# Optimization experiments

Hardware: AMD Instinct MI355X
Metric: run time of the kernel (lower is better)

Reference implementation:

```python
import jax, jax.numpy as jnp
import numpy as np

N_NODES = 50000  # 4 node types x 12500
N_PER = 12500
E = 600000
H = 128
IN_DIMS = [128, 128, 64, 64]


def setup_inputs() -> dict:
    key = jax.random.key(0)
    ks = jax.random.split(key, 16)
    inp = {}
    for i, d in enumerate(IN_DIMS):
        inp[f"feat{i}"] = jax.random.normal(ks[i], (N_PER, d), dtype=jnp.float32)
        # xavier_normal-ish init, gain 1.414
        std = 1.414 * np.sqrt(2.0 / (d + H))
        inp[f"W_fc{i}"] = jax.random.normal(ks[4 + i], (d, H), dtype=jnp.float32) * std
        inp[f"b_fc{i}"] = jnp.zeros((H,), dtype=jnp.float32)
    inp["src"] = jax.random.randint(ks[8], (E,), 0, N_NODES, dtype=jnp.int32)
    inp["dst"] = jax.random.randint(ks[9], (E,), 0, N_NODES, dtype=jnp.int32)
    inp["e_feat"] = jax.random.randint(ks[10], (E,), 0, 36, dtype=jnp.int32)
    inp["b_g0"] = jnp.zeros((H,), dtype=jnp.float32)  # GraphConv layer0 (weight=False, bias)
    inp["W_g1"] = jax.random.normal(ks[11], (H, H), dtype=jnp.float32) * np.sqrt(1.0 / H)
    inp["b_g1"] = jnp.zeros((H,), dtype=jnp.float32)
    return inp


def _degree_norms(src, dst):
    ones = jnp.ones((src.shape[0],), dtype=jnp.float32)
    deg_out = jax.ops.segment_sum(ones, src, num_segments=N_NODES)
    deg_in = jax.ops.segment_sum(ones, dst, num_segments=N_NODES)
    # DGL norm='both': D_out^{-1/2} on src side, D_in^{-1/2} on dst side (clamp 0-degree)
    out_norm = jax.lax.rsqrt(jnp.maximum(deg_out, 1.0))
    in_norm = jax.lax.rsqrt(jnp.maximum(deg_in, 1.0))
    return out_norm, in_norm


def _gcn_aggregate(h, src, dst, out_norm, in_norm):
    m = (h * out_norm[:, None])[src]                      # [E, H] gather
    agg = jax.ops.segment_sum(m, dst, num_segments=N_NODES)
    return agg * in_norm[:, None]


def reference(feat0, feat1, feat2, feat3,
              W_fc0, b_fc0, W_fc1, b_fc1, W_fc2, b_fc2, W_fc3, b_fc3,
              src, dst, e_feat, b_g0, W_g1, b_g1):
    # per-node-type linear projections, then concat along node dim
    h = jnp.concatenate([
        feat0 @ W_fc0 + b_fc0,
        feat1 @ W_fc1 + b_fc1,
        feat2 @ W_fc2 + b_fc2,
        feat3 @ W_fc3 + b_fc3,
    ], axis=0)  # [N_NODES, H]

    out_norm, in_norm = _degree_norms(src, dst)
    # GraphConv layer 0: weight=False, bias, activation (dropout p=0 -> identity)
    h = jax.nn.relu(_gcn_aggregate(h, src, dst, out_norm, in_norm) + b_g0)
    # GraphConv layer 1: aggregate, then linear weight + bias, activation
    h = jax.nn.relu(_gcn_aggregate(h, src, dst, out_norm, in_norm) @ W_g1 + b_g1)

    e = e_feat.astype(jnp.float32)  # e_feat.reshape(-1,1).float() in original
    # forward graph: msg = ft + sum_{r in 0..4} where(e==r, ft, 0) = ft * (1 + 1{e in 0..4})
    w_fwd = 1.0 + sum((e == float(r)).astype(jnp.float32) for r in (0, 1, 2, 3, 4))
    agg_a = jax.ops.segment_sum(h[src] * w_fwd[:, None], dst, num_segments=N_NODES)
    # transpose graph (reversed edges, same e): msg = sum_{r in {6,14,30}} where(e==r, ft, 0)
    w_bwd = sum((e == float(r)).astype(jnp.float32) for r in (6, 14, 30))
    agg_b = jax.ops.segment_sum(h[dst] * w_bwd[:, None], src, num_segments=N_NODES)
    return agg_a + agg_b
```

## Files before the change

kernel.cpp:

```cpp
#include <hip/hip_runtime.h>
#include <hip/hip_bf16.h>

#define N_NODES 50000
#define N_PER   12500
#define E_EDGES 600000
#define HDIM    128

#define NBLK_FC    ((N_PER + 63) / 64)
#define NBLK_NODE  ((N_NODES + 255) / 256)
#define MASK31  0x7fffffff

#define HQD 64
#define HSL_D (E_EDGES / HQD)
#define NBLK_DB (HQD * 4)

typedef __attribute__((ext_vector_type(8))) short bfrag;
typedef __attribute__((ext_vector_type(4))) float ffrag;

__device__ __forceinline__ unsigned short f2bf(float f) {
    union { float f; unsigned u; } x; x.f = f;
    unsigned r = x.u + 0x7fffu + ((x.u >> 16) & 1u);
    return (unsigned short)(r >> 16);
}
__device__ __forceinline__ float lo_bf(unsigned v) { return __uint_as_float(v << 16); }
__device__ __forceinline__ float hi_bf(unsigned v) { return __uint_as_float(v & 0xffff0000u); }
__device__ __forceinline__ unsigned pack2(float a, float b) {
    return (unsigned)f2bf(a) | ((unsigned)f2bf(b) << 16);
}
__device__ __forceinline__ float onrm_of(int deg) {
    return rsqrtf(fmaxf((float)deg, 1.0f));
}

__device__ __forceinline__ void acc8_add(float* acc, uint4 v) {
    acc[0] += lo_bf(v.x); acc[1] += hi_bf(v.x);
    acc[2] += lo_bf(v.y); acc[3] += hi_bf(v.y);
    acc[4] += lo_bf(v.z); acc[5] += hi_bf(v.z);
    acc[6] += lo_bf(v.w); acc[7] += hi_bf(v.w);
}
__device__ __forceinline__ void acc8_addw(float* acc, uint4 v, float w) {
    acc[0] += lo_bf(v.x) * w; acc[1] += hi_bf(v.x) * w;
    acc[2] += lo_bf(v.y) * w; acc[3] += hi_bf(v.y) * w;
    acc[4] += lo_bf(v.z) * w; acc[5] += hi_bf(v.z) * w;
    acc[6] += lo_bf(v.w) * w; acc[7] += hi_bf(v.w) * w;
}

__global__ __launch_bounds__(1024) void prep_kernel(
    const float* __restrict__ W0, const float* __restrict__ W1,
    const float* __restrict__ W2, const float* __restrict__ W3,
    const float* __restrict__ Wg,
    const int* __restrict__ src, const int* __restrict__ dst,
    const int* __restrict__ ef,
    unsigned short* __restrict__ Wp,
    unsigned short* __restrict__ partialS,
    unsigned short* __restrict__ partialD,
    unsigned char*  __restrict__ partialB) {
    __shared__ unsigned hist[N_PER];
    int b = blockIdx.x;
    if (b < NBLK_DB) {
        const int q = b >> 2;
        const int p = b & 3;
        const int g0 = p * N_PER;
        for (int j = threadIdx.x; j < N_PER; j += 1024) hist[j] = 0;
        __syncthreads();
        const int e0 = q * HSL_D;
        for (int i = e0 + threadIdx.x; i < e0 + HSL_D; i += 1024) {
            int d = dst[i], t = ef[i], s = src[i];
            unsigned rd = (unsigned)(d - g0);
            if (rd < (unsigned)N_PER) atomicAdd(&hist[rd], 1u);
            unsigned rs = (unsigned)(s - g0);
            if (rs < (unsigned)N_PER) {
                unsigned inc = 0x10000u
                             + ((t == 6 || t == 14 || t == 30) ? 0x400u : 0u);
                atomicAdd(&hist[rs], inc);
            }
        }
        __syncthreads();
        for (int j = threadIdx.x; j < N_PER; j += 1024) {
            unsigned h = hist[j];
            partialD[(size_t)q * N_NODES + g0 + j] = (unsigned short)(h & 0x3FFu);
            partialB[(size_t)q * N_NODES + g0 + j] = (unsigned char)((h >> 10) & 0x3Fu);
            partialS[(size_t)q * N_NODES + g0 + j] = (unsigned short)(h >> 16);
        }
    } else {
        int tid = (b - NBLK_DB) * 1024 + threadIdx.x;
        const float* W; int D, base, off;
        if      (tid < 2048) { W = W0; D = 128; base = 0;    off = 0;     }
        else if (tid < 4096) { W = W1; D = 128; base = 2048; off = 16384; }
        else if (tid < 5120) { W = W2; D = 64;  base = 4096; off = 32768; }
        else if (tid < 6144) { W = W3; D = 64;  base = 5120; off = 40960; }
        else                 { W = Wg; D = 128; base = 6144; off = 49152; }
        int t2 = tid - base;
        int KT = D / 32;
        int l = t2 & 63;
        int tt = t2 >> 6;
        int kt = tt % KT, n0 = tt / KT;
        int n = n0 * 16 + (l & 15);
        int kb = kt * 32 + (l >> 4) * 8;
#pragma unroll
        for (int j = 0; j < 8; ++j)
            Wp[(size_t)off + (size_t)t2 * 8 + j] = f2bf(W[(size_t)(kb + j) * 128 + n]);
    }
}

__global__ __launch_bounds__(256) void plane_prefix_kernel(
    unsigned short* __restrict__ partialD, unsigned char* __restrict__ partialB,
    const unsigned short* __restrict__ partialS,
    int* __restrict__ degD, int* __restrict__ degB,
    int* __restrict__ scanD, int* __restrict__ scanB,
    int* __restrict__ blocksumD, int* __restrict__ blocksumB,
    float* __restrict__ onrm_buf) {
    const int t = threadIdx.x;
    const int n = blockIdx.x * 256 + t;
    int dD = 0, dB = 0;
    if (n < N_NODES) {
        int run = 0;
#pragma unroll
        for (int q = 0; q < HQD; ++q) {
            size_t ix = (size_t)q * N_NODES + n;
            int c = partialD[ix];
            partialD[ix] = (unsigned short)run;
            run += c;
        }
        dD = run; degD[n] = run;
        run = 0;
#pragma unroll
        for (int q = 0; q < HQD; ++q) {
            size_t ix = (size_t)q * N_NODES + n;
            int c = partialB[ix];
            partialB[ix] = (unsigned char)run;
            run += c;
        }
        dB = run; degB[n] = run;
        int dS = 0;
#pragma unroll
        for (int q = 0; q < HQD; ++q)
            dS += partialS[(size_t)q * N_NODES + n];
        onrm_buf[n] = onrm_of(dS);
    }
    __shared__ int sD[256], sB[256];
    sD[t] = dD; sB[t] = dB;
    __syncthreads();
    for (int off = 1; off < 256; off <<= 1) {
        int xD = (t >= off) ? sD[t - off] : 0;
        int xB = (t >= off) ? sB[t - off] : 0;
        __syncthreads();
        sD[t] += xD; sB[t] += xB;
        __syncthreads();
    }
    if (n < N_NODES) {
        scanD[n] = sD[t] - dD;
        scanB[n] = sB[t] - dB;
    }
    if (t == 255) {
        blocksumD[blockIdx.x] = sD[255];
        blocksumB[blockIdx.x] = sB[255];
    }
}

__global__ __launch_bounds__(256) void base_add_kernel(
    const int* __restrict__ blocksumD, const int* __restrict__ blocksumB,
    int* __restrict__ scanD, int* __restrict__ scanB) {
    __shared__ int sD[256], sB[256];
    const int t = threadIdx.x;
    const int bid = blockIdx.x;
    sD[t] = (t < bid) ? blocksumD[t] : 0;
    sB[t] = (t < bid) ? blocksumB[t] : 0;
    __syncthreads();
    for (int off = 128; off >= 1; off >>= 1) {
        if (t < off) { sD[t] += sD[t + off]; sB[t] += sB[t + off]; }
        __syncthreads();
    }
    const int n = bid * 256 + t;
    if (n < N_NODES) { scanD[n] += sD[0]; scanB[n] += sB[0]; }
}

template<int D>
__device__ __forceinline__ void fc_body(
    int blk, int tid,
    const float* __restrict__ X,
    const unsigned short* __restrict__ Wp,
    const float* __restrict__ bias,
    const float* __restrict__ onrm,
    unsigned short* __restrict__ outbf,
    int rows)
{
    constexpr int KT = D / 32;
    const int lane = tid & 63;
    const int wave = tid >> 6;
    const int m = lane & 15, q = lane >> 4;
    const int rbase = blk * 64 + wave * 16;
    const int row = rbase + m;

    bfrag afr[KT];
#pragma unroll
    for (int kt = 0; kt < KT; ++kt) {
        bfrag a;
        if (row < rows) {
            const float* xp = X + (size_t)row * D + kt * 32 + q * 8;
            float4 u0 = *(const float4*)xp;
            float4 u1 = *(const float4*)(xp + 4);
            a[0] = (short)f2bf(u0.x); a[1] = (short)f2bf(u0.y);
            a[2] = (short)f2bf(u0.z); a[3] = (short)f2bf(u0.w);
            a[4] = (short)f2bf(u1.x); a[5] = (short)f2bf(u1.y);
            a[6] = (short)f2bf(u1.z); a[7] = (short)f2bf(u1.w);
        } else {
#pragma unroll
            for (int t = 0; t < 8; ++t) a[t] = 0;
        }
        afr[kt] = a;
    }

    ffrag acc[8];
#pragma unroll
    for (int n0 = 0; n0 < 8; ++n0)
#pragma unroll
        for (int t = 0; t < 4; ++t) acc[n0][t] = 0.f;

#pragma unroll
    for (int n0 = 0; n0 < 8; ++n0)
#pragma unroll
        for (int kt = 0; kt < KT; ++kt) {
            bfrag bfr = *(const bfrag*)(Wp + ((size_t)(n0 * KT + kt) * 64 + lane) * 8);
            acc[n0] = __builtin_amdgcn_mfma_f32_16x16x32_bf16(afr[kt], bfr, acc[n0], 0, 0, 0);
        }

#pragma unroll
    for (int n0 = 0; n0 < 8; ++n0) {
        const int col = n0 * 16 + m;
        const float bj = bias[col];
#pragma unroll
        for (int r = 0; r < 4; ++r) {
            int orow = rbase + q * 4 + r;
            if (orow < rows)
                outbf[(size_t)orow * 128 + col] =
                    f2bf((acc[n0][r] + bj) * onrm[orow]);
        }
    }
}

__global__ __launch_bounds__(1024) void scatfc_kernel(
    const int* __restrict__ src, const int* __restrict__ dst,
    const int* __restrict__ ef,
    const unsigned short* __restrict__ prefD,
    const unsigned char*  __restrict__ prefB,
    const int* __restrict__ scanD, const int* __restrict__ scanB,
    int* __restrict__ bucket, int* __restrict__ bucketB,
    const float* __restrict__ f0, const float* __restrict__ f1,
    const float* __restrict__ f2, const float* __restrict__ f3,
    const unsigned short* __restrict__ Wp,
    const float* __restrict__ b0, const float* __restrict__ b1,
    const float* __restrict__ b2, const float* __restrict__ b3,
    const float* __restrict__ onrm_buf,
    unsigned short* __restrict__ Abf)
{
    __shared__ unsigned offP[N_PER];
    const int b = blockIdx.x;
    if (b < NBLK_DB) {
        const int q = b >> 2;
        const int p = b & 3;
        const int g0 = p * N_PER;
        for (int j = threadIdx.x; j < N_PER; j += 1024)
            offP[j] = (unsigned)(scanD[g0 + j] + (int)prefD[(size_t)q * N_NODES + g0 + j])
                    | ((unsigned)prefB[(size_t)q * N_NODES + g0 + j] << 20);
        __syncthreads();
        const int e0 = q * HSL_D;
        for (int i = e0 + threadIdx.x; i < e0 + HSL_D; i += 1024) {
            int s = src[i], d = dst[i], t = ef[i];
            unsigned rd = (unsigned)(d - g0);
            if (rd < (unsigned)N_PER) {
                unsigned old = atomicAdd(&offP[rd], 1u);
                bucket[old & 0xFFFFFu] = s | ((t <= 4) ? 0x80000000 : 0);
            }
            if (t == 6 || t == 14 || t == 30) {
                unsigned rs = (unsigned)(s - g0);
                if (rs < (unsigned)N_PER) {
                    unsigned old = atomicAdd(&offP[rs], 1u << 20);
                    bucketB[scanB[s] + (int)(old >> 20)] = d;
                }
            }
        }
    } else {
        int ft = (b - NBLK_DB) * 4 + (threadIdx.x >> 8);
        int tid = threadIdx.x & 255;
        int which = ft / NBLK_FC;
        int blk = ft - which * NBLK_FC;
        if (which == 0)
            fc_body<128>(blk, tid, f0, Wp,         b0, onrm_buf,
                         Abf + (size_t)0 * N_PER * HDIM, N_PER);
        else if (which == 1)
            fc_body<128>(blk, tid, f1, Wp + 16384, b1, onrm_buf + N_PER,
                         Abf + (size_t)1 * N_PER * HDIM, N_PER);
        else if (which == 2)
            fc_body<64>(blk, tid, f2, Wp + 32768, b2, onrm_buf + 2 * N_PER,
                        Abf + (size_t)2 * N_PER * HDIM, N_PER);
        else
            fc_body<64>(blk, tid, f3, Wp + 40960, b3, onrm_buf + 3 * N_PER,
                        Abf + (size_t)3 * N_PER * HDIM, N_PER);
    }
}

__global__ __launch_bounds__(256) void agg0g_kernel(
    const uint4* __restrict__ A,
    const int* __restrict__ bucket, const int* __restrict__ scanD,
    const int* __restrict__ degD,
    const float* __restrict__ onrm_buf, const float* __restrict__ b_g0,
    const unsigned short* __restrict__ Wp,
    unsigned short* __restrict__ BW) {
    __shared__ uint4 Bt[256];
    const int tdx = threadIdx.x;
    const int nloc = tdx >> 4, j8 = tdx & 15;
    const int n = blockIdx.x * 16 + nloc;

    const int cnt = degD[n];
    const int* bk = bucket + scanD[n];
    float acc[8] = {0.f, 0.f, 0.f, 0.f, 0.f, 0.f, 0.f, 0.f};
    int i = 0;
    for (; i + 8 <= cnt; i += 8) {
        uint4 v[8];
#pragma unroll
        for (int k = 0; k < 8; ++k)
            v[k] = A[(size_t)(bk[i + k] & MASK31) * 16 + j8];
#pragma unroll
        for (int k = 0; k < 8; ++k) acc8_add(acc, v[k]);
    }
    if (i + 4 <= cnt) {
        uint4 v[4];
#pragma unroll
        for (int k = 0; k < 4; ++k)
            v[k] = A[(size_t)(bk[i + k] & MASK31) * 16 + j8];
#pragma unroll
        for (int k = 0; k < 4; ++k) acc8_add(acc, v[k]);
        i += 4;
    }
    for (; i < cnt; ++i)
        acc8_add(acc, A[(size_t)(bk[i] & MASK31) * 16 + j8]);

    float inr = onrm_of(cnt);
    float onr = onrm_buf[n];
    const float* bg = b_g0 + j8 * 8;
    float r[8];
#pragma unroll
    for (int k = 0; k < 8; ++k)
        r[k] = fmaxf(acc[k] * inr + bg[k], 0.f) * onr;
    uint4 o;
    o.x = pack2(r[0], r[1]); o.y = pack2(r[2], r[3]);
    o.z = pack2(r[4], r[5]); o.w = pack2(r[6], r[7]);
    Bt[j8 * 16 + nloc] = o;
    __syncthreads();

    const int lane = tdx & 63;
    const int wave = tdx >> 6;
    const int m = lane & 15, q = lane >> 4;

    bfrag afr[4];
#pragma unroll
    for (int kt = 0; kt < 4; ++kt)
        afr[kt] = *(const bfrag*)(Bt + (kt * 4 + q) * 16 + m);

    ffrag acc2[2];
#pragma unroll
    for (int t2 = 0; t2 < 2; ++t2) {
#pragma unroll
        for (int t = 0; t < 4; ++t) acc2[t2][t] = 0.f;
        const int n0 = wave * 2 + t2;
#pragma unroll
        for (int kt = 0; kt < 4; ++kt) {
            bfrag bfr = *(const bfrag*)(Wp + ((size_t)(n0 * 4 + kt) * 64 + lane) * 8);
            acc2[t2] = __builtin_amdgcn_mfma_f32_16x16x32_bf16(afr[kt], bfr, acc2[t2], 0, 0, 0);
        }
    }

    const int rowbase = blockIdx.x * 16;
#pragma unroll
    for (int t2 = 0; t2 < 2; ++t2) {
        const int col = (wave * 2 + t2) * 16 + m;
#pragma unroll
        for (int rr = 0; rr < 4; ++rr) {
            const int row = rowbase + q * 4 + rr;
            BW[(size_t)row * 128 + col] = f2bf(acc2[t2][rr]);
        }
    }
}

__global__ __launch_bounds__(256) void agg1_kernel(
    const uint4* __restrict__ BW,
    const int* __restrict__ bucket, const int* __restrict__ scanD,
    const int* __restrict__ degD,
    const float* __restrict__ b_g1,
    uint4* __restrict__ H) {
    int idx = blockIdx.x * blockDim.x + threadIdx.x;
    int n = idx >> 4, j8 = idx & 15;
    const int cnt = degD[n];
    const int* bk = bucket + scanD[n];
    float acc[8] = {0.f, 0.f, 0.f, 0.f, 0.f, 0.f, 0.f, 0.f};
    int i = 0;
    for (; i + 8 <= cnt; i += 8) {
        uint4 v[8];
#pragma unroll
        for (int k = 0; k < 8; ++k)
            v[k] = BW[(size_t)(bk[i + k] & MASK31) * 16 + j8];
#pragma unroll
        for (int k = 0; k < 8; ++k) acc8_add(acc, v[k]);
    }
    if (i + 4 <= cnt) {
        uint4 v[4];
#pragma unroll
        for (int k = 0; k < 4; ++k)
            v[k] = BW[(size_t)(bk[i + k] & MASK31) * 16 + j8];
#pragma unroll
        for (int k = 0; k < 4; ++k) acc8_add(acc, v[k]);
        i += 4;
    }
    for (; i < cnt; ++i)
        acc8_add(acc, BW[(size_t)(bk[i] & MASK31) * 16 + j8]);
    float inr = onrm_of(cnt);
    const float* bg = b_g1 + j8 * 8;
    float r[8];
#pragma unroll
    for (int k = 0; k < 8; ++k)
        r[k] = fmaxf(acc[k] * inr + bg[k], 0.f);
    uint4 o;
    o.x = pack2(r[0], r[1]); o.y = pack2(r[2], r[3]);
    o.z = pack2(r[4], r[5]); o.w = pack2(r[6], r[7]);
    H[(size_t)n * 16 + j8] = o;
}

__global__ __launch_bounds__(256) void final_kernel(
    const uint4* __restrict__ H,
    const int* __restrict__ bucket, const int* __restrict__ scanD,
    const int* __restrict__ degD,
    const int* __restrict__ bucketB, const int* __restrict__ scanB,
    const int* __restrict__ degB,
    float4* __restrict__ out4) {
    int idx = blockIdx.x * blockDim.x + threadIdx.x;
    int n = idx >> 4, j8 = idx & 15;
    float acc[8] = {0.f, 0.f, 0.f, 0.f, 0.f, 0.f, 0.f, 0.f};
    const int cnt = degD[n];
    const int* bk = bucket + scanD[n];
    int i = 0;
    for (; i + 8 <= cnt; i += 8) {
        int c[8]; uint4 v[8];
#pragma unroll
        for (int k = 0; k < 8; ++k) c[k] = bk[i + k];
#pragma unroll
        for (int k = 0; k < 8; ++k)
            v[k] = H[(size_t)(c[k] & MASK31) * 16 + j8];
#pragma unroll
        for (int k = 0; k < 8; ++k)
            acc8_addw(acc, v[k], (c[k] < 0) ? 2.0f : 1.0f);
    }
    if (i + 4 <= cnt) {
        int c[4]; uint4 v[4];
#pragma unroll
        for (int k = 0; k < 4; ++k) c[k] = bk[i + k];
#pragma unroll
        for (int k = 0; k < 4; ++k)
            v[k] = H[(size_t)(c[k] & MASK31) * 16 + j8];
#pragma unroll
        for (int k = 0; k < 4; ++k)
            acc8_addw(acc, v[k], (c[k] < 0) ? 2.0f : 1.0f);
        i += 4;
    }
    for (; i < cnt; ++i) {
        int c = bk[i];
        acc8_addw(acc, H[(size_t)(c & MASK31) * 16 + j8], (c < 0) ? 2.0f : 1.0f);
    }
    const int cb = degB[n];
    const int* bkB = bucketB + scanB[n];
    for (int k = 0; k < cb; ++k) {
        int d = bkB[k];
        acc8_add(acc, H[(size_t)d * 16 + j8]);
    }
    float4 o0 = {acc[0], acc[1], acc[2], acc[3]};
    float4 o1 = {acc[4], acc[5], acc[6], acc[7]};
    out4[(size_t)n * 32 + j8 * 2]     = o0;
    out4[(size_t)n * 32 + j8 * 2 + 1] = o1;
}

extern "C" void kernel_launch(void* const* d_in, const int* in_sizes, int n_in,
                              void* d_out, int out_size, void* d_ws, size_t ws_size,
                              hipStream_t stream) {
    const float* feat[4]  = {(const float*)d_in[0], (const float*)d_in[3],
                             (const float*)d_in[6], (const float*)d_in[9]};
    const float* W_fc[4]  = {(const float*)d_in[1], (const float*)d_in[4],
                             (const float*)d_in[7], (const float*)d_in[10]};
    const float* b_fc[4]  = {(const float*)d_in[2], (const float*)d_in[5],
                             (const float*)d_in[8], (const float*)d_in[11]};
    const int*   src      = (const int*)d_in[12];
    const int*   dst      = (const int*)d_in[13];
    const int*   efeat    = (const int*)d_in[14];
    const float* b_g0     = (const float*)d_in[15];
    const float* W_g1     = (const float*)d_in[16];
    const float* b_g1     = (const float*)d_in[17];
    float* out = (float*)d_out;

    char* p = (char*)d_ws;
    unsigned short* Abf = (unsigned short*)p; p += (size_t)N_NODES * HDIM * 2;
    unsigned short* Bbf = (unsigned short*)p; p += (size_t)N_NODES * HDIM * 2;
    unsigned short* Wp  = (unsigned short*)p; p += (size_t)65536 * 2;
    int* bucket  = (int*)p; p += (size_t)E_EDGES * 4;
    int* bucketB = (int*)p; p += (size_t)E_EDGES * 4;
    unsigned short* partialS = (unsigned short*)p; p += (size_t)HQD * N_NODES * 2;
    unsigned short* partialD = (unsigned short*)p; p += (size_t)HQD * N_NODES * 2;
    unsigned char*  partialB = (unsigned char*)p;  p += (size_t)HQD * N_NODES;
    int* degD  = (int*)p; p += (size_t)N_NODES * 4;
    int* degB  = (int*)p; p += (size_t)N_NODES * 4;
    int* scanD = (int*)p; p += (size_t)N_NODES * 4;
    int* scanB = (int*)p; p += (size_t)N_NODES * 4;
    float* onrm_buf = (float*)p; p += (size_t)N_NODES * 4;
    int* blocksumD = (int*)p; p += 256 * 4;
    int* blocksumB = (int*)p; p += 256 * 4;

    const unsigned short* Wpg = Wp + 49152;

    prep_kernel<<<NBLK_DB + 8, 1024, 0, stream>>>(
        W_fc[0], W_fc[1], W_fc[2], W_fc[3], W_g1, src, dst, efeat,
        Wp, partialS, partialD, partialB);

    plane_prefix_kernel<<<NBLK_NODE, 256, 0, stream>>>(
        partialD, partialB, partialS, degD, degB, scanD, scanB,
        blocksumD, blocksumB, onrm_buf);

    base_add_kernel<<<NBLK_NODE, 256, 0, stream>>>(
        blocksumD, blocksumB, scanD, scanB);

    scatfc_kernel<<<NBLK_DB + NBLK_FC, 1024, 0, stream>>>(
        src, dst, efeat, partialD, partialB, scanD, scanB, bucket, bucketB,
        feat[0], feat[1], feat[2], feat[3], Wp,
        b_fc[0], b_fc[1], b_fc[2], b_fc[3], onrm_buf, Abf);

    const int grid_node = (N_NODES * 16) / 256;

    agg0g_kernel<<<grid_node, 256, 0, stream>>>(
        (const uint4*)Abf, bucket, scanD, degD, onrm_buf, b_g0, Wpg,
        Bbf);

    agg1_kernel<<<grid_node, 256, 0, stream>>>(
        (const uint4*)Bbf, bucket, scanD, degD, b_g1, (uint4*)Abf);

    final_kernel<<<grid_node, 256, 0, stream>>>(
        (const uint4*)Abf, bucket, scanD, degD, bucketB, scanB, degB, (float4*)out);
}
```

Measured before the change: 233.6 us.

## Pack degree-count planes into one word and pad CSR rows for vector index loads

Merges the three per-quarter histogram planes (dst count, backward count, src count) into a single 32-bit word array, so the prefix kernel reads and writes one plane instead of three. Pads each dst CSR row start to a multiple of four so the aggregation kernels can load neighbor indices as int4 vectors, and packs (offset, degree) into an int2 per node. The cost is a larger bucket buffer plus extra csr arrays, and the padded offsets rely on the alignment being kept consistent everywhere.

```diff
diff --git a/kernel.cpp b/kernel.cpp
--- a/kernel.cpp
+++ b/kernel.cpp
@@ -51,9 +51,7 @@
     const int* __restrict__ src, const int* __restrict__ dst,
     const int* __restrict__ ef,
     unsigned short* __restrict__ Wp,
-    unsigned short* __restrict__ partialS,
-    unsigned short* __restrict__ partialD,
-    unsigned char*  __restrict__ partialB) {
+    unsigned* __restrict__ partial) {
     __shared__ unsigned hist[N_PER];
     int b = blockIdx.x;
     if (b < NBLK_DB) {
@@ -75,12 +73,8 @@
             }
         }
         __syncthreads();
-        for (int j = threadIdx.x; j < N_PER; j += 1024) {
-            unsigned h = hist[j];
-            partialD[(size_t)q * N_NODES + g0 + j] = (unsigned short)(h & 0x3FFu);
-            partialB[(size_t)q * N_NODES + g0 + j] = (unsigned char)((h >> 10) & 0x3Fu);
-            partialS[(size_t)q * N_NODES + g0 + j] = (unsigned short)(h >> 16);
-        }
+        for (int j = threadIdx.x; j < N_PER; j += 1024)
+            partial[(size_t)q * N_NODES + g0 + j] = hist[j];
     } else {
         int tid = (b - NBLK_DB) * 1024 + threadIdx.x;
         const float* W; int D, base, off;
@@ -103,42 +97,32 @@
 }
 
 __global__ __launch_bounds__(256) void plane_prefix_kernel(
-    unsigned short* __restrict__ partialD, unsigned char* __restrict__ partialB,
-    const unsigned short* __restrict__ partialS,
+    unsigned* __restrict__ partial,
     int* __restrict__ degD, int* __restrict__ degB,
     int* __restrict__ scanD, int* __restrict__ scanB,
     int* __restrict__ blocksumD, int* __restrict__ blocksumB,
     float* __restrict__ onrm_buf) {
     const int t = threadIdx.x;
     const int n = blockIdx.x * 256 + t;
-    int dD = 0, dB = 0;
+    int dA = 0, dD = 0, dB = 0;
     if (n < N_NODES) {
-        int run = 0;
+        int runD = 0, runB = 0, dS = 0;
 #pragma unroll
         for (int q = 0; q < HQD; ++q) {
             size_t ix = (size_t)q * N_NODES + n;
-            int c = partialD[ix];
-            partialD[ix] = (unsigned short)run;
-            run += c;
-        }
-        dD = run; degD[n] = run;
-        run = 0;
-#pragma unroll
-        for (int q = 0; q < HQD; ++q) {
-            size_t ix = (size_t)q * N_NODES + n;
-            int c = partialB[ix];
-            partialB[ix] = (unsigned char)run;
-            run += c;
-        }
-        dB = run; degB[n] = run;
-        int dS = 0;
-#pragma unroll
-        for (int q = 0; q < HQD; ++q)
-            dS += partialS[(size_t)q * N_NODES + n];
+            unsigned w = partial[ix];
+            partial[ix] = (unsigned)runD | ((unsigned)runB << 10);
+            runD += (int)(w & 0x3FFu);
+            runB += (int)((w >> 10) & 0x3Fu);
+            dS   += (int)(w >> 16);
+        }
+        dD = runD; dB = runB;
+        degD[n] = dD; degB[n] = dB;
         onrm_buf[n] = onrm_of(dS);
+        dA = (dD + 3) & ~3;
     }
     __shared__ int sD[256], sB[256];
-    sD[t] = dD; sB[t] = dB;
+    sD[t] = dA; sB[t] = dB;
     __syncthreads();
     for (int off = 1; off < 256; off <<= 1) {
         int xD = (t >= off) ? sD[t - off] : 0;
@@ -148,7 +132,7 @@
         __syncthreads();
     }
     if (n < N_NODES) {
-        scanD[n] = sD[t] - dD;
+        scanD[n] = sD[t] - dA;
         scanB[n] = sB[t] - dB;
     }
     if (t == 255) {
@@ -159,7 +143,9 @@
 
 __global__ __launch_bounds__(256) void base_add_kernel(
     const int* __restrict__ blocksumD, const int* __restrict__ blocksumB,
-    int* __restrict__ scanD, int* __restrict__ scanB) {
+    const int* __restrict__ scanD, const int* __restrict__ scanB,
+    const int* __restrict__ degD, const int* __restrict__ degB,
+    int2* __restrict__ csrD, int2* __restrict__ csrB) {
     __shared__ int sD[256], sB[256];
     const int t = threadIdx.x;
     const int bid = blockIdx.x;
@@ -171,7 +157,10 @@
         __syncthreads();
     }
     const int n = bid * 256 + t;
-    if (n < N_NODES) { scanD[n] += sD[0]; scanB[n] += sB[0]; }
+    if (n < N_NODES) {
+        csrD[n] = make_int2(scanD[n] + sD[0], degD[n]);
+        csrB[n] = make_int2(scanB[n] + sB[0], degB[n]);
+    }
 }
 
 template<int D>
@@ -241,9 +230,8 @@
 __global__ __launch_bounds__(1024) void scatfc_kernel(
     const int* __restrict__ src, const int* __restrict__ dst,
     const int* __restrict__ ef,
-    const unsigned short* __restrict__ prefD,
-    const unsigned char*  __restrict__ prefB,
-    const int* __restrict__ scanD, const int* __restrict__ scanB,
+    const unsigned* __restrict__ partial,
+    const int2* __restrict__ csrD, const int2* __restrict__ csrB,
     int* __restrict__ bucket, int* __restrict__ bucketB,
     const float* __restrict__ f0, const float* __restrict__ f1,
     const float* __restrict__ f2, const float* __restrict__ f3,
@@ -259,9 +247,11 @@
         const int q = b >> 2;
         const int p = b & 3;
         const int g0 = p * N_PER;
-        for (int j = threadIdx.x; j < N_PER; j += 1024)
-            offP[j] = (unsigned)(scanD[g0 + j] + (int)prefD[(size_t)q * N_NODES + g0 + j])
-                    | ((unsigned)prefB[(size_t)q * N_NODES + g0 + j] << 20);
+        for (int j = threadIdx.x; j < N_PER; j += 1024) {
+            unsigned w = partial[(size_t)q * N_NODES + g0 + j];
+            offP[j] = (unsigned)(csrD[g0 + j].x + (int)(w & 0x3FFu))
+                    | (((w >> 10) & 0x3Fu) << 20);
+        }
         __syncthreads();
         const int e0 = q * HSL_D;
         for (int i = e0 + threadIdx.x; i < e0 + HSL_D; i += 1024) {
@@ -275,7 +265,7 @@
                 unsigned rs = (unsigned)(s - g0);
                 if (rs < (unsigned)N_PER) {
                     unsigned old = atomicAdd(&offP[rs], 1u << 20);
-                    bucketB[scanB[s] + (int)(old >> 20)] = d;
+                    bucketB[csrB[s].x + (int)(old >> 20)] = d;
                 }
             }
         }
@@ -299,10 +289,35 @@
     }
 }
 
+#define GATHER8(DSTARR)                                                       \
+    for (; i + 8 <= cnt; i += 8) {                                            \
+        int4 c0 = *(const int4*)(bk + i);                                     \
+        int4 c1 = *(const int4*)(bk + i + 4);                                 \
+        int cc[8] = {c0.x, c0.y, c0.z, c0.w, c1.x, c1.y, c1.z, c1.w};         \
+        uint4 v[8];                                                           \
+        _Pragma("unroll")                                                     \
+        for (int k = 0; k < 8; ++k)                                           \
+            v[k] = DSTARR[(size_t)(cc[k] & MASK31) * 16 + j8];                \
+        _Pragma("unroll")                                                     \
+        for (int k = 0; k < 8; ++k) acc8_add(acc, v[k]);                      \
+    }                                                                         \
+    if (i + 4 <= cnt) {                                                       \
+        int4 c0 = *(const int4*)(bk + i);                                     \
+        int cc[4] = {c0.x, c0.y, c0.z, c0.w};                                 \
+        uint4 v[4];                                                           \
+        _Pragma("unroll")                                                     \
+        for (int k = 0; k < 4; ++k)                                           \
+            v[k] = DSTARR[(size_t)(cc[k] & MASK31) * 16 + j8];                \
+        _Pragma("unroll")                                                     \
+        for (int k = 0; k < 4; ++k) acc8_add(acc, v[k]);                      \
+        i += 4;                                                               \
+    }                                                                         \
+    for (; i < cnt; ++i)                                                      \
+        acc8_add(acc, DSTARR[(size_t)(bk[i] & MASK31) * 16 + j8]);
+
 __global__ __launch_bounds__(256) void agg0g_kernel(
     const uint4* __restrict__ A,
-    const int* __restrict__ bucket, const int* __restrict__ scanD,
-    const int* __restrict__ degD,
+    const int* __restrict__ bucket, const int2* __restrict__ csrD,
     const float* __restrict__ onrm_buf, const float* __restrict__ b_g0,
     const unsigned short* __restrict__ Wp,
     unsigned short* __restrict__ BW) {
@@ -311,29 +326,12 @@
     const int nloc = tdx >> 4, j8 = tdx & 15;
     const int n = blockIdx.x * 16 + nloc;
 
-    const int cnt = degD[n];
-    const int* bk = bucket + scanD[n];
+    const int2 cd = csrD[n];
+    const int cnt = cd.y;
+    const int* bk = bucket + cd.x;
     float acc[8] = {0.f, 0.f, 0.f, 0.f, 0.f, 0.f, 0.f, 0.f};
     int i = 0;
-    for (; i + 8 <= cnt; i += 8) {
-        uint4 v[8];
-#pragma unroll
-        for (int k = 0; k < 8; ++k)
-            v[k] = A[(size_t)(bk[i + k] & MASK31) * 16 + j8];
-#pragma unroll
-        for (int k = 0; k < 8; ++k) acc8_add(acc, v[k]);
-    }
-    if (i + 4 <= cnt) {
-        uint4 v[4];
-#pragma unroll
-        for (int k = 0; k < 4; ++k)
-            v[k] = A[(size_t)(bk[i + k] & MASK31) * 16 + j8];
-#pragma unroll
-        for (int k = 0; k < 4; ++k) acc8_add(acc, v[k]);
-        i += 4;
-    }
-    for (; i < cnt; ++i)
-        acc8_add(acc, A[(size_t)(bk[i] & MASK31) * 16 + j8]);
+    GATHER8(A)
 
     float inr = onrm_of(cnt);
     float onr = onrm_buf[n];
@@ -384,35 +382,17 @@
 
 __global__ __launch_bounds__(256) void agg1_kernel(
     const uint4* __restrict__ BW,
-    const int* __restrict__ bucket, const int* __restrict__ scanD,
-    const int* __restrict__ degD,
+    const int* __restrict__ bucket, const int2* __restrict__ csrD,
     const float* __restrict__ b_g1,
     uint4* __restrict__ H) {
     int idx = blockIdx.x * blockDim.x + threadIdx.x;
     int n = idx >> 4, j8 = idx & 15;
-    const int cnt = degD[n];
-    const int* bk = bucket + scanD[n];
+    const int2 cd = csrD[n];
+    const int cnt = cd.y;
+    const int* bk = bucket + cd.x;
     float acc[8] = {0.f, 0.f, 0.f, 0.f, 0.f, 0.f, 0.f, 0.f};
     int i = 0;
-    for (; i + 8 <= cnt; i += 8) {
-        uint4 v[8];
-#pragma unroll
-        for (int k = 0; k < 8; ++k)
-            v[k] = BW[(size_t)(bk[i + k] & MASK31) * 16 + j8];
-#pragma unroll
-        for (int k = 0; k < 8; ++k) acc8_add(acc, v[k]);
-    }
-    if (i + 4 <= cnt) {
-        uint4 v[4];
-#pragma unroll
-        for (int k = 0; k < 4; ++k)
-            v[k] = BW[(size_t)(bk[i + k] & MASK31) * 16 + j8];
-#pragma unroll
-        for (int k = 0; k < 4; ++k) acc8_add(acc, v[k]);
-        i += 4;
-    }
-    for (; i < cnt; ++i)
-        acc8_add(acc, BW[(size_t)(bk[i] & MASK31) * 16 + j8]);
+    GATHER8(BW)
     float inr = onrm_of(cnt);
     const float* bg = b_g1 + j8 * 8;
     float r[8];
@@ -427,50 +407,48 @@
 
 __global__ __launch_bounds__(256) void final_kernel(
     const uint4* __restrict__ H,
-    const int* __restrict__ bucket, const int* __restrict__ scanD,
-    const int* __restrict__ degD,
-    const int* __restrict__ bucketB, const int* __restrict__ scanB,
-    const int* __restrict__ degB,
+    const int* __restrict__ bucket, const int2* __restrict__ csrD,
+    const int* __restrict__ bucketB, const int2* __restrict__ csrB,
     float4* __restrict__ out4) {
     int idx = blockIdx.x * blockDim.x + threadIdx.x;
     int n = idx >> 4, j8 = idx & 15;
     float acc[8] = {0.f, 0.f, 0.f, 0.f, 0.f, 0.f, 0.f, 0.f};
-    const int cnt = degD[n];
-    const int* bk = bucket + scanD[n];
+    const int2 cd = csrD[n];
+    const int cnt = cd.y;
+    const int* bk = bucket + cd.x;
     int i = 0;
     for (; i + 8 <= cnt; i += 8) {
-        int c[8]; uint4 v[8];
-#pragma unroll
-        for (int k = 0; k < 8; ++k) c[k] = bk[i + k];
+        int4 c0 = *(const int4*)(bk + i);
+        int4 c1 = *(const int4*)(bk + i + 4);
+        int cc[8] = {c0.x, c0.y, c0.z, c0.w, c1.x, c1.y, c1.z, c1.w};
+        uint4 v[8];
 #pragma unroll
         for (int k = 0; k < 8; ++k)
-            v[k] = H[(size_t)(c[k] & MASK31) * 16 + j8];
+            v[k] = H[(size_t)(cc[k] & MASK31) * 16 + j8];
 #pragma unroll
         for (int k = 0; k < 8; ++k)
-            acc8_addw(acc, v[k], (c[k] < 0) ? 2.0f : 1.0f);
+            acc8_addw(acc, v[k], (cc[k] < 0) ? 2.0f : 1.0f);
     }
     if (i + 4 <= cnt) {
-        int c[4]; uint4 v[4];
-#pragma unroll
-        for (int k = 0; k < 4; ++k) c[k] = bk[i + k];
+        int4 c0 = *(const int4*)(bk + i);
+        int cc[4] = {c0.x, c0.y, c0.z, c0.w};
+        uint4 v[4];
 #pragma unroll
         for (int k = 0; k < 4; ++k)
-            v[k] = H[(size_t)(c[k] & MASK31) * 16 + j8];
+            v[k] = H[(size_t)(cc[k] & MASK31) * 16 + j8];
 #pragma unroll
         for (int k = 0; k < 4; ++k)
-            acc8_addw(acc, v[k], (c[k] < 0) ? 2.0f : 1.0f);
+            acc8_addw(acc, v[k], (cc[k] < 0) ? 2.0f : 1.0f);
         i += 4;
     }
     for (; i < cnt; ++i) {
         int c = bk[i];
         acc8_addw(acc, H[(size_t)(c & MASK31) * 16 + j8], (c < 0) ? 2.0f : 1.0f);
     }
-    const int cb = degB[n];
-    const int* bkB = bucketB + scanB[n];
-    for (int k = 0; k < cb; ++k) {
-        int d = bkB[k];
-        acc8_add(acc, H[(size_t)d * 16 + j8]);
-    }
+    const int2 cb = csrB[n];
+    const int* bkB = bucketB + cb.x;
+    for (int k = 0; k < cb.y; ++k)
+        acc8_add(acc, H[(size_t)bkB[k] * 16 + j8]);
     float4 o0 = {acc[0], acc[1], acc[2], acc[3]};
     float4 o1 = {acc[4], acc[5], acc[6], acc[7]};
     out4[(size_t)n * 32 + j8 * 2]     = o0;
@@ -498,15 +476,15 @@
     unsigned short* Abf = (unsigned short*)p; p += (size_t)N_NODES * HDIM * 2;
     unsigned short* Bbf = (unsigned short*)p; p += (size_t)N_NODES * HDIM * 2;
     unsigned short* Wp  = (unsigned short*)p; p += (size_t)65536 * 2;
-    int* bucket  = (int*)p; p += (size_t)E_EDGES * 4;
+    int* bucket  = (int*)p; p += (size_t)(E_EDGES + 4 * N_NODES) * 4;
     int* bucketB = (int*)p; p += (size_t)E_EDGES * 4;
-    unsigned short* partialS = (unsigned short*)p; p += (size_t)HQD * N_NODES * 2;
-    unsigned short* partialD = (unsigned short*)p; p += (size_t)HQD * N_NODES * 2;
-    unsigned char*  partialB = (unsigned char*)p;  p += (size_t)HQD * N_NODES;
+    unsigned* partial = (unsigned*)p; p += (size_t)HQD * N_NODES * 4;
     int* degD  = (int*)p; p += (size_t)N_NODES * 4;
     int* degB  = (int*)p; p += (size_t)N_NODES * 4;
     int* scanD = (int*)p; p += (size_t)N_NODES * 4;
     int* scanB = (int*)p; p += (size_t)N_NODES * 4;
+    int2* csrD = (int2*)p; p += (size_t)N_NODES * 8;
+    int2* csrB = (int2*)p; p += (size_t)N_NODES * 8;
     float* onrm_buf = (float*)p; p += (size_t)N_NODES * 4;
     int* blocksumD = (int*)p; p += 256 * 4;
     int* blocksumB = (int*)p; p += 256 * 4;
@@ -515,29 +493,27 @@
 
     prep_kernel<<<NBLK_DB + 8, 1024, 0, stream>>>(
         W_fc[0], W_fc[1], W_fc[2], W_fc[3], W_g1, src, dst, efeat,
-        Wp, partialS, partialD, partialB);
+        Wp, partial);
 
     plane_prefix_kernel<<<NBLK_NODE, 256, 0, stream>>>(
-        partialD, partialB, partialS, degD, degB, scanD, scanB,
-        blocksumD, blocksumB, onrm_buf);
+        partial, degD, degB, scanD, scanB, blocksumD, blocksumB, onrm_buf);
 
     base_add_kernel<<<NBLK_NODE, 256, 0, stream>>>(
-        blocksumD, blocksumB, scanD, scanB);
+        blocksumD, blocksumB, scanD, scanB, degD, degB, csrD, csrB);
 
     scatfc_kernel<<<NBLK_DB + NBLK_FC, 1024, 0, stream>>>(
-        src, dst, efeat, partialD, partialB, scanD, scanB, bucket, bucketB,
+        src, dst, efeat, partial, csrD, csrB, bucket, bucketB,
         feat[0], feat[1], feat[2], feat[3], Wp,
         b_fc[0], b_fc[1], b_fc[2], b_fc[3], onrm_buf, Abf);
 
     const int grid_node = (N_NODES * 16) / 256;
 
     agg0g_kernel<<<grid_node, 256, 0, stream>>>(
-        (const uint4*)Abf, bucket, scanD, degD, onrm_buf, b_g0, Wpg,
-        Bbf);
+        (const uint4*)Abf, bucket, csrD, onrm_buf, b_g0, Wpg, Bbf);
 
     agg1_kernel<<<grid_node, 256, 0, stream>>>(
-        (const uint4*)Bbf, bucket, scanD, degD, b_g1, (uint4*)Abf);
+        (const uint4*)Bbf, bucket, csrD, b_g1, (uint4*)Abf);
 
     final_kernel<<<grid_node, 256, 0, stream>>>(
-        (const uint4*)Abf, bucket, scanD, degD, bucketB, scanB, degB, (float4*)out);
-}
+        (const uint4*)Abf, bucket, csrD, bucketB, csrB, (float4*)out);
+}
```

After: 226.2 us. 1.03x faster.
